# Kernel optimization log

Measured on AMD Instinct MI355X. Metric: run time of the kernel, lower is better.

## Reference

```python
import jax, jax.numpy as jnp
from jax import lax
import numpy as np

B, F_IN, S = 8, 64, 8192
HID = 256
F_OUT_MLP = 64
OUT = 64
D_COMB = F_IN + 2 * F_OUT_MLP  # 192
MAX_K = 200
EPS = 1e-8


def _ema_channels(x_flat, halflife):
    # x_flat: (BF, S); halflife: (BF,). Causal truncated-window EMA, faithful to
    # the torch grouped conv1d (weight alpha**lag over last K samples, normalized).
    BF, Slen = x_flat.shape
    K = min(MAX_K + 1, Slen)
    alpha = 0.5 ** (1.0 / halflife)                      # (BF,)
    lags = jnp.arange(K, dtype=x_flat.dtype)[::-1]       # K-1 .. 0
    kernel = alpha[:, None] ** lags[None, :]             # (BF, K), kernel[i]=alpha^(K-1-i)
    dn = ('NCH', 'OIH', 'NCH')
    conv = lambda inp: lax.conv_general_dilated(
        inp[None], kernel[:, None, :], (1,), [(K - 1, 0)],
        feature_group_count=BF, dimension_numbers=dn)[0]
    num = conv(x_flat)
    den = conv(jnp.ones_like(x_flat))
    return num / (den + EPS)


def _adaptive_ema(x, log_halflife):
    # x: (B, F, S); per-feature halflife broadcast over batch, like torch expand+flatten
    Bb, Ff, Ss = x.shape
    hl = jnp.tile(jnp.exp(log_halflife), Bb)             # (B*F,)
    return _ema_channels(x.reshape(Bb * Ff, Ss), hl).reshape(Bb, Ff, Ss)


def _featurewise_mlp(x, W1, b1, W2, b2):
    # x: (B, F, S) -> per-token MLP with ReLU
    Bb, Ff, Ss = x.shape
    xt = x.transpose(0, 2, 1).reshape(Bb * Ss, Ff)
    y = jax.nn.relu(xt @ W1 + b1) @ W2 + b2
    return y.reshape(Bb, Ss, -1).transpose(0, 2, 1)


def setup_inputs() -> dict:
    key = jax.random.key(0)
    ks = jax.random.split(key, 8)
    lo, hi = float(np.log(4.0)), float(np.log(256.0))
    u = lambda k, n: jax.random.uniform(k, (n,)) * (hi - lo) + lo
    return {
        'x': jax.random.normal(ks[0], (B, F_IN, S), dtype=jnp.float32),
        'log_hl_in': u(ks[1], F_IN),
        'log_hl_out': u(ks[2], F_OUT_MLP),
        'log_hl_var': u(ks[3], F_IN),
        'W1': jax.random.normal(ks[4], (F_IN, HID)) / np.sqrt(F_IN).astype(np.float32),
        'b1': jnp.zeros((HID,), jnp.float32),
        'W2': jax.random.normal(ks[5], (HID, F_OUT_MLP)) / np.sqrt(HID).astype(np.float32),
        'b2': jnp.zeros((F_OUT_MLP,), jnp.float32),
        'norm_w': jnp.ones((D_COMB,), jnp.float32),
        'lin_W': jax.random.normal(ks[6], (D_COMB, 2 * OUT)) / np.sqrt(D_COMB).astype(np.float32),
        'lin_b': jnp.zeros((2 * OUT,), jnp.float32),
    }


def reference(x, log_hl_in, log_hl_out, log_hl_var, W1, b1, W2, b2, norm_w, lin_W, lin_b):
    Bb, _, Ss = x.shape
    ema_mlp = _adaptive_ema(_featurewise_mlp(x, W1, b1, W2, b2), log_hl_out)
    mlp_ema = _featurewise_mlp(_adaptive_ema(x, log_hl_in), W1, b1, W2, b2)
    ema_var = _adaptive_ema(x * x, log_hl_var) - _adaptive_ema(x, log_hl_var) ** 2
    # NOTE: original code multiplies the first two branches by 0 before concat
    combined = jnp.concatenate([ema_mlp * 0, mlp_ema * 0, ema_var], axis=1)  # (B, D_COMB, S)
    cf = combined.transpose(0, 2, 1).reshape(Bb * Ss, D_COMB)
    rms = jnp.sqrt(jnp.mean(cf * cf, axis=-1, keepdims=True) + EPS)
    cn = cf / rms * norm_w
    lin_out = cn @ lin_W + lin_b                          # (B*S, 2*OUT)
    skip_flat, out_flat = lin_out[:, :OUT], lin_out[:, OUT:]
    skip_y = skip_flat.reshape(Bb, Ss, -1).transpose(0, 2, 1)
    output = out_flat.reshape(Bb, Ss, -1).transpose(0, 2, 1)
    return (output, skip_y)
```

## Files before the change

kernel.cpp:

```cpp
#include <hip/hip_runtime.h>
#include <math.h>


#define SB    8192
#define BB    8
#define FF    64
#define EPSF  1e-8f
#define HALO  201

#define PAD1(o) ((o) + ((o) >> 5))
#define QLEN (PAD1(SB - 1) + 1)

__global__ __launch_bounds__(256) void ema_var_kernel(
    const float* __restrict__ x,
    const float* __restrict__ log_hl_var,
    float* __restrict__ var_out)
{
  __shared__ float qx [QLEN];
  __shared__ float qx2[QLEN];
  __shared__ float wcx[4], wcx2[4];

  const int tid  = threadIdx.x;
  const int lane = tid & 63;
  const int w    = tid >> 6;
  const int bf   = blockIdx.x;
  const int b    = bf >> 6;
  const int f    = bf & 63;

  const float hl     = expf(log_hl_var[f]);
  const float invhl  = 1.0f / hl;
  const float alpha  = exp2f(-invhl);
  const float a201   = exp2f(-201.0f * invhl);
  const float inv1ma = 1.0f / (1.0f - alpha);
  const float rd_st  = 1.0f / ((1.0f - a201) * inv1ma + EPSF);
  const float m32    = exp2f(-32.0f * invhl);
  const float m2048  = exp2f(-2048.0f * invhl);

  const float* __restrict__ xp = x + (long)(b * FF + f) * SB;
  const int t0 = tid * 32;

  float qa[32];
  float q2[32];
#pragma unroll
  for (int g = 0; g < 8; ++g) {
    const float4 v4 = *(const float4*)&xp[t0 + g * 4];
    qa[g*4+0] = v4.x; qa[g*4+1] = v4.y; qa[g*4+2] = v4.z; qa[g*4+3] = v4.w;
  }

  {
    float sx = 0.f, sx2 = 0.f;
#pragma unroll
    for (int j = 0; j < 32; ++j) {
      const float xv = qa[j];
      sx  = fmaf(alpha, sx,  xv);
      sx2 = fmaf(alpha, sx2, xv * xv);
      qa[j] = sx;
      q2[j] = sx2;
    }
  }

  float bx = qa[31], bx2 = q2[31];
  {
    float p = m32;
#pragma unroll
    for (int off = 1; off < 64; off <<= 1) {
      const float ux  = __shfl_up(bx,  off, 64);
      const float ux2 = __shfl_up(bx2, off, 64);
      if (lane >= off) { bx = fmaf(p, ux, bx); bx2 = fmaf(p, ux2, bx2); }
      p *= p;
    }
  }
  if (lane == 63) { wcx[w] = bx; wcx2[w] = bx2; }
  __syncthreads();

  float ax = 0.f, ax2 = 0.f;
  for (int i = 0; i < w; ++i) {
    ax  = fmaf(m2048, ax,  wcx[i]);
    ax2 = fmaf(m2048, ax2, wcx2[i]);
  }

  const float bux  = __shfl_up(bx,  1, 64);
  const float bux2 = __shfl_up(bx2, 1, 64);
  const float powl = exp2f(-32.0f * (float)lane * invhl);
  float Cx, Cx2;
  if (lane == 0) { Cx = ax;                  Cx2 = ax2; }
  else           { Cx = fmaf(powl, ax, bux); Cx2 = fmaf(powl, ax2, bux2); }

  {
    float pf = alpha;
    const int base = 33 * tid;
#pragma unroll
    for (int j = 0; j < 32; ++j) {
      const float qv  = fmaf(pf, Cx,  qa[j]);
      const float qv2 = fmaf(pf, Cx2, q2[j]);
      qa[j] = qv;  q2[j] = qv2;
      qx [base + j] = qv;
      qx2[base + j] = qv2;
      pf *= alpha;
    }
  }
  __syncthreads();

  float vr[32];
#pragma unroll
  for (int j = 0; j < 32; ++j) {
    const int t = t0 + j;
    float nqx = qa[j], nqx2 = q2[j];
    if (t >= HALO) {
      const int po = PAD1(t - HALO);
      nqx  = fmaf(-a201, qx [po], nqx);
      nqx2 = fmaf(-a201, qx2[po], nqx2);
    }
    float rd = rd_st;
    if (t < 200) {
      rd = 1.0f / ((1.0f - exp2f(-(float)(t + 1) * invhl)) * inv1ma + EPSF);
    }
    const float m1 = nqx * rd;
    vr[j] = fmaf(nqx2, rd, -(m1 * m1));
  }
  __syncthreads();

  {
    const int base = 33 * tid;
#pragma unroll
    for (int j = 0; j < 32; ++j) qx[base + j] = vr[j];
  }
  __syncthreads();

  float* __restrict__ vp = var_out + (long)(b * FF + f) * SB;
#pragma unroll
  for (int g = 0; g < 8; ++g) {
    const int i = (g * 256 + tid) * 4;
    float4 v4;
    v4.x = qx[PAD1(i + 0)];
    v4.y = qx[PAD1(i + 1)];
    v4.z = qx[PAD1(i + 2)];
    v4.w = qx[PAD1(i + 3)];
    *(float4*)&vp[i] = v4;
  }
}

#define RT 256

__global__ __launch_bounds__(512, 2) void stage2_kernel(
    const float* __restrict__ var,
    const float* __restrict__ norm_w,
    const float* __restrict__ lin_W,
    const float* __restrict__ lin_b,
    float* __restrict__ out)
{
  __shared__ float vt[FF * RT];
  __shared__ float invl[RT];

  const int tid = threadIdx.x;
  const int b   = blockIdx.x >> 5;
  const int t0  = (blockIdx.x & 31) * RT;

  const int lane = tid & 63;
  const int w    = tid >> 6;

  {
    const float* __restrict__ vbase = var + (long)(b * FF) * SB + t0;
#pragma unroll
    for (int f = w; f < FF; f += 8) {
      float4 v4 = *(const float4*)&vbase[(long)f * SB + lane * 4];
      *(float4*)&vt[f * RT + lane * 4] = v4;
    }
  }
  __syncthreads();

  if (tid < RT) {
    float ss = 0.f;
#pragma unroll
    for (int f = 0; f < FF; ++f) {
      const float v = vt[f * RT + tid];
      ss = fmaf(v, v, ss);
    }
    invl[tid] = 1.0f / sqrtf(fmaf(ss, (1.0f / 192.0f), EPSF));
  }
  __syncthreads();

  const int tt = lane;
  const int k0 = __builtin_amdgcn_readfirstlane(w * 16);

  const float* __restrict__ wbase = lin_W + 128 * 128 + k0;
  const float* __restrict__ nwb   = norm_w + 128;

  float acc[4][16];
#pragma unroll
  for (int j = 0; j < 4; ++j)
#pragma unroll
    for (int kk = 0; kk < 16; ++kk) acc[j][kk] = 0.f;

  for (int f = 0; f < FF; ++f) {
    const float4 va = *(const float4*)&vt[f * RT + tt * 4];
    const float nwf = nwb[f];
    const float4 w0 = *(const float4*)&wbase[f * 128 + 0];
    const float4 w1 = *(const float4*)&wbase[f * 128 + 4];
    const float4 w2 = *(const float4*)&wbase[f * 128 + 8];
    const float4 w3 = *(const float4*)&wbase[f * 128 + 12];
    const float wv[16] = { w0.x, w0.y, w0.z, w0.w, w1.x, w1.y, w1.z, w1.w,
                           w2.x, w2.y, w2.z, w2.w, w3.x, w3.y, w3.z, w3.w };
    const float vv[4] = { va.x * nwf, va.y * nwf, va.z * nwf, va.w * nwf };
#pragma unroll
    for (int j = 0; j < 4; ++j)
#pragma unroll
      for (int kk = 0; kk < 16; ++kk)
        acc[j][kk] = fmaf(vv[j], wv[kk], acc[j][kk]);
  }

  const float4 inv4 = *(const float4*)&invl[tt * 4];
  const float iv[4] = { inv4.x, inv4.y, inv4.z, inv4.w };
  const long skip_base = (long)BB * 64 * SB;

#pragma unroll
  for (int kk = 0; kk < 16; ++kk) {
    const int k = k0 + kk;
    const float bk = lin_b[k];
    float4 r;
    r.x = fmaf(acc[0][kk], iv[0], bk);
    r.y = fmaf(acc[1][kk], iv[1], bk);
    r.z = fmaf(acc[2][kk], iv[2], bk);
    r.w = fmaf(acc[3][kk], iv[3], bk);
    const long dst = (k < 64)
        ? (skip_base + ((long)(b * 64 + k)) * SB + t0 + tt * 4)
        : (((long)(b * 64 + (k - 64))) * SB + t0 + tt * 4);
    *(float4*)&out[dst] = r;
  }
}

extern "C" void kernel_launch(void* const* d_in, const int* in_sizes, int n_in,
                              void* d_out, int out_size, void* d_ws, size_t ws_size,
                              hipStream_t stream) {
  const float* x          = (const float*)d_in[0];
  const float* log_hl_var = (const float*)d_in[3];
  const float* norm_w     = (const float*)d_in[8];
  const float* lin_W      = (const float*)d_in[9];
  const float* lin_b      = (const float*)d_in[10];
  float* var_ws = (float*)d_ws;
  float* out    = (float*)d_out;

  ema_var_kernel<<<dim3(BB * FF), dim3(256), 0, stream>>>(x, log_hl_var, var_ws);
  stage2_kernel<<<dim3(BB * (SB / RT)), dim3(512), 0, stream>>>(
      var_ws, norm_w, lin_W, lin_b, out);
}
```

Before: 121.6 us.

## Halve stage2 row tile, raise occupancy, parallelize RMS reduction across threads

The stage2 kernel now handles 128 time steps per block instead of 256, which doubles the grid and halves shared memory per block. Each thread computes 2 time steps by 16 outputs instead of 4 by 16, cutting register use so launch bounds can request 4 blocks per CU. The sum-of-squares for the RMS norm is split across all 512 threads in four partial groups, then combined, instead of using only 256 threads serially. The trade-offs are narrower float2 global stores, more repeated weight loads per output, and an extra barrier.

```diff
diff --git a/kernel.cpp b/kernel.cpp
--- a/kernel.cpp
+++ b/kernel.cpp
@@ -140,9 +140,9 @@
   }
 }
 
-#define RT 256
-
-__global__ __launch_bounds__(512, 2) void stage2_kernel(
+#define RT 128
+
+__global__ __launch_bounds__(512, 4) void stage2_kernel(
     const float* __restrict__ var,
     const float* __restrict__ norm_w,
     const float* __restrict__ lin_W,
@@ -150,50 +150,59 @@
     float* __restrict__ out)
 {
   __shared__ float vt[FF * RT];
+  __shared__ float part[4 * RT];
   __shared__ float invl[RT];
 
   const int tid = threadIdx.x;
-  const int b   = blockIdx.x >> 5;
-  const int t0  = (blockIdx.x & 31) * RT;
+  const int b   = blockIdx.x >> 6;
+  const int t0g = (blockIdx.x & 63) * RT;
 
   const int lane = tid & 63;
   const int w    = tid >> 6;
 
   {
-    const float* __restrict__ vbase = var + (long)(b * FF) * SB + t0;
-#pragma unroll
-    for (int f = w; f < FF; f += 8) {
-      float4 v4 = *(const float4*)&vbase[(long)f * SB + lane * 4];
-      *(float4*)&vt[f * RT + lane * 4] = v4;
-    }
-  }
-  __syncthreads();
-
+    const float* __restrict__ vbase = var + (long)(b * FF) * SB + t0g;
+#pragma unroll
+    for (int s = 0; s < 4; ++s) {
+      const int fi = s * 512 + tid;
+      const int f  = fi >> 5;
+      const int c  = (fi & 31) * 4;
+      float4 v4 = *(const float4*)&vbase[(long)f * SB + c];
+      *(float4*)&vt[f * RT + c] = v4;
+    }
+  }
+  __syncthreads();
+
+  {
+    const int t  = tid & 127;
+    const int fg = tid >> 7;
+    float ss = 0.f;
+#pragma unroll
+    for (int f = fg * 16; f < fg * 16 + 16; ++f) {
+      const float v = vt[f * RT + t];
+      ss = fmaf(v, v, ss);
+    }
+    part[fg * RT + t] = ss;
+  }
+  __syncthreads();
   if (tid < RT) {
-    float ss = 0.f;
-#pragma unroll
-    for (int f = 0; f < FF; ++f) {
-      const float v = vt[f * RT + tid];
-      ss = fmaf(v, v, ss);
-    }
+    const float ss = part[tid] + part[RT + tid] + part[2 * RT + tid] + part[3 * RT + tid];
     invl[tid] = 1.0f / sqrtf(fmaf(ss, (1.0f / 192.0f), EPSF));
   }
   __syncthreads();
 
-  const int tt = lane;
+  const int t0 = lane * 2;
   const int k0 = __builtin_amdgcn_readfirstlane(w * 16);
 
   const float* __restrict__ wbase = lin_W + 128 * 128 + k0;
   const float* __restrict__ nwb   = norm_w + 128;
 
-  float acc[4][16];
-#pragma unroll
-  for (int j = 0; j < 4; ++j)
-#pragma unroll
-    for (int kk = 0; kk < 16; ++kk) acc[j][kk] = 0.f;
+  float acc0[16], acc1[16];
+#pragma unroll
+  for (int kk = 0; kk < 16; ++kk) { acc0[kk] = 0.f; acc1[kk] = 0.f; }
 
   for (int f = 0; f < FF; ++f) {
-    const float4 va = *(const float4*)&vt[f * RT + tt * 4];
+    const float2 va = *(const float2*)&vt[f * RT + t0];
     const float nwf = nwb[f];
     const float4 w0 = *(const float4*)&wbase[f * 128 + 0];
     const float4 w1 = *(const float4*)&wbase[f * 128 + 4];
@@ -201,31 +210,30 @@
     const float4 w3 = *(const float4*)&wbase[f * 128 + 12];
     const float wv[16] = { w0.x, w0.y, w0.z, w0.w, w1.x, w1.y, w1.z, w1.w,
                            w2.x, w2.y, w2.z, w2.w, w3.x, w3.y, w3.z, w3.w };
-    const float vv[4] = { va.x * nwf, va.y * nwf, va.z * nwf, va.w * nwf };
-#pragma unroll
-    for (int j = 0; j < 4; ++j)
-#pragma unroll
-      for (int kk = 0; kk < 16; ++kk)
-        acc[j][kk] = fmaf(vv[j], wv[kk], acc[j][kk]);
-  }
-
-  const float4 inv4 = *(const float4*)&invl[tt * 4];
-  const float iv[4] = { inv4.x, inv4.y, inv4.z, inv4.w };
+    const float vv0 = va.x * nwf;
+    const float vv1 = va.y * nwf;
+#pragma unroll
+    for (int kk = 0; kk < 16; ++kk) {
+      acc0[kk] = fmaf(vv0, wv[kk], acc0[kk]);
+      acc1[kk] = fmaf(vv1, wv[kk], acc1[kk]);
+    }
+  }
+
+  const float iv0 = invl[t0];
+  const float iv1 = invl[t0 + 1];
   const long skip_base = (long)BB * 64 * SB;
 
 #pragma unroll
   for (int kk = 0; kk < 16; ++kk) {
     const int k = k0 + kk;
     const float bk = lin_b[k];
-    float4 r;
-    r.x = fmaf(acc[0][kk], iv[0], bk);
-    r.y = fmaf(acc[1][kk], iv[1], bk);
-    r.z = fmaf(acc[2][kk], iv[2], bk);
-    r.w = fmaf(acc[3][kk], iv[3], bk);
+    float2 r;
+    r.x = fmaf(acc0[kk], iv0, bk);
+    r.y = fmaf(acc1[kk], iv1, bk);
     const long dst = (k < 64)
-        ? (skip_base + ((long)(b * 64 + k)) * SB + t0 + tt * 4)
-        : (((long)(b * 64 + (k - 64))) * SB + t0 + tt * 4);
-    *(float4*)&out[dst] = r;
+        ? (skip_base + ((long)(b * 64 + k)) * SB + t0g + t0)
+        : (((long)(b * 64 + (k - 64))) * SB + t0g + t0);
+    *(float2*)&out[dst] = r;
   }
 }
 
```

After: 117.1 us. 1.04x faster.
